# Kernel optimization log

Measured on AMD Instinct MI355X. Metric: run time of the kernel, lower is better.

## Reference

```python
import jax, jax.numpy as jnp
import numpy as np

N_HEAD = 16
D_MODEL = 1024
D_HEAD = 64
B = 2
S = 2048      # query length
M = 512       # memory length
K = S + M     # key length
L = 2 * K - 1 # relative position table length
SCALE = 1.0 / np.sqrt(D_MODEL)  # NOTE: module scales by 1/sqrt(d_model), not d_head
EPS = 1e-5


def layer_norm(x, gamma, beta):
    mu = jnp.mean(x, axis=-1, keepdims=True)
    var = jnp.mean(jnp.square(x - mu), axis=-1, keepdims=True)
    return (x - mu) * jax.lax.rsqrt(var + EPS) * gamma + beta


def skew(qpos, mem_len):
    # qpos: (B, H, S, 2K-1) -> relative-position scores aligned to keys (B, H, S, K)
    b, h, s, l = qpos.shape
    k_len = (l + 1) // 2
    pad = jnp.full((b, h, s, 1), -jnp.inf, dtype=qpos.dtype)
    rel = jnp.concatenate([qpos, pad], axis=-1)          # (B,H,S,2K)
    rel = rel.reshape(b, h, s * (l + 1))[..., : s * l]    # drop tail, shift rows
    rel = rel.reshape(b, h, s, l)
    start = (k_len - 1) - mem_len
    return rel[..., start : start + k_len]


def setup_inputs() -> dict:
    key = jax.random.key(0)
    ks = jax.random.split(key, 8)
    w_scale = 1.0 / np.sqrt(D_MODEL)
    hidden = jax.random.normal(ks[0], (B, S, D_MODEL), jnp.float32)
    memory = jax.random.normal(ks[1], (B, M, D_MODEL), jnp.float32)
    pos_emb = jax.random.normal(ks[2], (B, L, D_HEAD), jnp.float32)
    Wq = jax.random.normal(ks[3], (D_MODEL, N_HEAD * D_HEAD), jnp.float32) * w_scale
    Wk = jax.random.normal(ks[4], (D_MODEL, N_HEAD * D_HEAD), jnp.float32) * w_scale
    Wv = jax.random.normal(ks[5], (D_MODEL, N_HEAD * D_HEAD), jnp.float32) * w_scale
    Wo = jax.random.normal(ks[6], (N_HEAD * D_HEAD, D_MODEL), jnp.float32) * w_scale
    gamma = jnp.ones((D_MODEL,), jnp.float32)
    beta = jnp.zeros((D_MODEL,), jnp.float32)
    # causal mask with memory: query i may attend keys j <= i + M; True = drop
    i = jnp.arange(S)[:, None]
    j = jnp.arange(K)[None, :]
    mask = j > (i + M)  # (S, K) bool
    return {"hidden": hidden, "pos_emb": pos_emb, "memory": memory,
            "Wq": Wq, "Wk": Wk, "Wv": Wv, "Wo": Wo,
            "gamma": gamma, "beta": beta, "mask": mask}


def reference(hidden, pos_emb, memory, Wq, Wk, Wv, Wo, gamma, beta, mask):
    combined = jnp.concatenate([memory, hidden], axis=1)  # (B, K, D)
    hn = layer_norm(hidden, gamma, beta)                  # pre_lnorm
    cn = layer_norm(combined, gamma, beta)
    q = (hn @ Wq).reshape(B, S, N_HEAD, D_HEAD).transpose(0, 2, 1, 3)  # (B,H,S,Dh)
    k = (cn @ Wk).reshape(B, K, N_HEAD, D_HEAD).transpose(0, 2, 1, 3)  # (B,H,K,Dh)
    v = (cn @ Wv).reshape(B, K, N_HEAD, D_HEAD).transpose(0, 2, 1, 3)  # (B,H,K,Dh)
    scores = jnp.einsum("bhsd,bhkd->bhsk", q, k)           # content term
    qpos = jnp.einsum("bhsd,bld->bhsl", q, pos_emb)        # position term (B,H,S,2K-1)
    scores = (scores + skew(qpos, M)) * SCALE
    scores = jnp.where(mask[None, None], -jnp.inf, scores)
    attn = jax.nn.softmax(scores, axis=-1)
    atten_vec = jnp.einsum("bhsk,bhkd->bshd", attn, v).reshape(B, S, N_HEAD * D_HEAD)
    output = atten_vec @ Wo
    # faithful quirk: residual uses the layer-normed hidden when pre_lnorm=True
    return hn + output
```

## Files before the change

### kernel.cpp

```cpp
#include <hip/hip_runtime.h>

typedef unsigned short u16;
typedef float f32x4 __attribute__((ext_vector_type(4)));
typedef short short8 __attribute__((ext_vector_type(8)));

#define MFMA_BF16(a, b, c) __builtin_amdgcn_mfma_f32_16x16x32_bf16((a), (b), (c), 0, 0, 0)

#define NEG_BIG (-30000.0f)

typedef __attribute__((address_space(1))) const void gas_void;
typedef __attribute__((address_space(3))) void las_void;

__device__ __forceinline__ float bf2f(u16 v) {
  union { unsigned int u; float f; } c; c.u = ((unsigned int)v) << 16; return c.f;
}
__device__ __forceinline__ u16 f2bf(float f) {
  union { float f; unsigned int u; } c; c.f = f;
  return (u16)((c.u + 0x7fffu + ((c.u >> 16) & 1u)) >> 16);
}

__global__ __launch_bounds__(256) void cast_pe_k(const float* __restrict__ src, u16* __restrict__ dst,
                                                 int n4, int* __restrict__ ctr) {
  const int idx = blockIdx.x * 256 + threadIdx.x;
  if (idx == 0) *ctr = 0;
  if (idx >= n4) return;
  const float4 d = *(const float4*)&src[idx * 4];
  ushort4 o;
  o.x = f2bf(d.x); o.y = f2bf(d.y); o.z = f2bf(d.z); o.w = f2bf(d.w);
  *(ushort4*)&dst[idx * 4] = o;
}

__global__ __launch_bounds__(256) void transpose_k(const float* __restrict__ W0, const float* __restrict__ W1,
                                                   const float* __restrict__ W2, const float* __restrict__ W3,
                                                   u16* __restrict__ Wt) {
  __shared__ float t[32][33];
  const float* W = (blockIdx.z == 0) ? W0 : (blockIdx.z == 1) ? W1 : (blockIdx.z == 2) ? W2 : W3;
  u16* dst = Wt + (size_t)blockIdx.z * 1024 * 1024;
  const int tx = threadIdx.x, ty = threadIdx.y;
  const int x0 = blockIdx.x * 32, y0 = blockIdx.y * 32;
#pragma unroll
  for (int i = 0; i < 32; i += 8)
    t[ty + i][tx] = W[(size_t)(y0 + ty + i) * 1024 + x0 + tx];
  __syncthreads();
#pragma unroll
  for (int i = 0; i < 32; i += 8)
    dst[(size_t)(x0 + ty + i) * 1024 + y0 + tx] = f2bf(t[tx][ty + i]);
}

__global__ __launch_bounds__(256) void ln_k(const float* __restrict__ hid, const float* __restrict__ mem,
                                            const float* __restrict__ gam, const float* __restrict__ bet,
                                            u16* __restrict__ cn) {
  const int row = blockIdx.x;
  const int b = (row >= 2560) ? 1 : 0;
  const int r = row - b * 2560;
  const float* src = (r < 512) ? (mem + ((size_t)b * 512 + r) * 1024)
                               : (hid + ((size_t)b * 2048 + (r - 512)) * 1024);
  const int tid = threadIdx.x;
  const float4 d = *(const float4*)&src[tid * 4];
  float x[4] = {d.x, d.y, d.z, d.w};
  float s = x[0] + x[1] + x[2] + x[3];
  float q = x[0]*x[0] + x[1]*x[1] + x[2]*x[2] + x[3]*x[3];
#pragma unroll
  for (int o = 1; o < 64; o <<= 1) { s += __shfl_xor(s, o); q += __shfl_xor(q, o); }
  __shared__ float sb[4], qsb[4];
  const int wave = tid >> 6;
  if ((tid & 63) == 0) { sb[wave] = s; qsb[wave] = q; }
  __syncthreads();
  s = sb[0] + sb[1] + sb[2] + sb[3];
  q = qsb[0] + qsb[1] + qsb[2] + qsb[3];
  const float mu = s * (1.0f / 1024.0f);
  const float var = q * (1.0f / 1024.0f) - mu * mu;
  const float rstd = rsqrtf(fmaxf(var, 0.0f) + 1e-5f);
  u16 o4[4];
#pragma unroll
  for (int i = 0; i < 4; ++i) {
    const int c = tid * 4 + i;
    o4[i] = f2bf((x[i] - mu) * rstd * gam[c] + bet[c]);
  }
  uint2 pk;
  pk.x = (unsigned)o4[0] | ((unsigned)o4[1] << 16);
  pk.y = (unsigned)o4[2] | ((unsigned)o4[3] << 16);
  *(uint2*)&cn[((size_t)b * 2560 + r) * 1024 + tid * 4] = pk;
}

__global__ __launch_bounds__(256, 3) void gemm128_k(const u16* __restrict__ A, const u16* __restrict__ Bt,
                                                    u16* __restrict__ qb, u16* __restrict__ kbo,
                                                    u16* __restrict__ vtb) {
  __shared__ u16 smem[16384];
  const int tid = threadIdx.x;
  const int lane = tid & 63, w = tid >> 6;
  const int quad = lane >> 4, l15 = lane & 15, r7 = l15 & 7;
  const int wr = w >> 1, wc = w & 1;
  const int row0 = blockIdx.y * 128, col0 = blockIdx.x * 128;
  const int rloc = w * 8 + (lane >> 3);
  const int cg = ((lane & 7) ^ ((lane >> 3) & 7)) * 8;
  const u16* ga = A + (size_t)(row0 + rloc) * 1024 + cg;
  const u16* gb = Bt + (size_t)(col0 + rloc) * 1024 + cg;
  f32x4 z = {0.f, 0.f, 0.f, 0.f};
  f32x4 acc[4][4];
#pragma unroll
  for (int m = 0; m < 4; ++m)
#pragma unroll
    for (int n = 0; n < 4; ++n) acc[m][n] = z;
  for (int kt = 0; kt < 16; ++kt) {
    const int k0 = kt * 64;
#pragma unroll
    for (int g2 = 0; g2 < 4; ++g2) {
      __builtin_amdgcn_global_load_lds((gas_void*)(ga + (size_t)g2 * 32 * 1024 + k0),
                                       (las_void*)(smem + (g2 * 32 + w * 8) * 64), 16, 0, 0);
      __builtin_amdgcn_global_load_lds((gas_void*)(gb + (size_t)g2 * 32 * 1024 + k0),
                                       (las_void*)(smem + 8192 + (g2 * 32 + w * 8) * 64), 16, 0, 0);
    }
    __syncthreads();
    short8 af0[4], af1[4];
#pragma unroll
    for (int m = 0; m < 4; ++m) {
      const int row = wr * 64 + m * 16 + l15;
      af0[m] = *(const short8*)&smem[row * 64 + (quad ^ r7) * 8];
      af1[m] = *(const short8*)&smem[row * 64 + ((quad + 4) ^ r7) * 8];
    }
#pragma unroll
    for (int n = 0; n < 4; ++n) {
      const int row = wc * 64 + n * 16 + l15;
      const short8 bf0 = *(const short8*)&smem[8192 + row * 64 + (quad ^ r7) * 8];
      const short8 bf1 = *(const short8*)&smem[8192 + row * 64 + ((quad + 4) ^ r7) * 8];
#pragma unroll
      for (int m = 0; m < 4; ++m) {
        acc[m][n] = MFMA_BF16(af0[m], bf0, acc[m][n]);
        acc[m][n] = MFMA_BF16(af1[m], bf1, acc[m][n]);
      }
    }
    __syncthreads();
  }
  const int nc = col0 >> 10;
  if (nc != 2) {
#pragma unroll
    for (int m = 0; m < 4; ++m) {
#pragma unroll
      for (int n = 0; n < 4; ++n) {
#pragma unroll
        for (int r = 0; r < 4; ++r) {
          const int R = row0 + wr * 64 + m * 16 + quad * 4 + r;
          const int C = col0 + wc * 64 + n * 16 + l15;
          const float v = acc[m][n][r];
          const int c = C & 1023, h = c >> 6, dh = c & 63;
          const int b = (R >= 2560) ? 1 : 0, kk = R - b * 2560;
          if (nc == 0) {
            if (kk >= 512)
              qb[(((size_t)(b * 16 + h)) * 2048 + (kk - 512)) * 64 + dh] = f2bf(v * 0.03125f);
          } else {
            kbo[(((size_t)(b * 16 + h)) * 2560 + kk) * 64 + dh] = f2bf(v);
          }
        }
      }
    }
  } else {
#pragma unroll
    for (int m = 0; m < 4; ++m)
#pragma unroll
      for (int n = 0; n < 4; ++n)
#pragma unroll
        for (int r = 0; r < 4; ++r) {
          const int rl = wr * 64 + m * 16 + quad * 4 + r;
          const int cl = wc * 64 + n * 16 + l15;
          smem[cl * 128 + (rl ^ ((cl & 7) << 3))] = f2bf(acc[m][n][r]);
        }
    __syncthreads();
    const int bb = (row0 >= 2560) ? 1 : 0;
    const int kk0 = row0 - bb * 2560;
#pragma unroll
    for (int half = 0; half < 2; ++half) {
      const int cl = (tid >> 2) + half * 64;
      const int c = (col0 - 2048) + cl;
      const int hh = c >> 6, dh = c & 63;
      u16* dst = &vtb[(((size_t)(bb * 16 + hh)) * 64 + dh) * 2560 + kk0];
#pragma unroll
      for (int inner = 0; inner < 4; ++inner) {
        const int rl = inner * 32 + (tid & 3) * 8;
        *(short8*)(dst + rl) = *(const short8*)&smem[cl * 128 + (rl ^ ((cl & 7) << 3))];
      }
    }
  }
}

__global__ __launch_bounds__(256, 3) void gemm_out_k(const u16* __restrict__ A, const u16* __restrict__ Bt,
                                                     float* __restrict__ outf,
                                                     const u16* __restrict__ resid) {
  __shared__ u16 smem[16384];
  const int tid = threadIdx.x;
  const int lane = tid & 63, w = tid >> 6;
  const int quad = lane >> 4, l15 = lane & 15, r7 = l15 & 7;
  const int wr = w >> 1, wc = w & 1;
  const int row0 = blockIdx.y * 128, col0 = blockIdx.x * 128;
  const int rloc = w * 8 + (lane >> 3);
  const int cg = ((lane & 7) ^ ((lane >> 3) & 7)) * 8;
  const u16* ga = A + (size_t)(row0 + rloc) * 1024 + cg;
  const u16* gb = Bt + (size_t)(col0 + rloc) * 1024 + cg;
  f32x4 z = {0.f, 0.f, 0.f, 0.f};
  f32x4 acc[4][4];
#pragma unroll
  for (int m = 0; m < 4; ++m)
#pragma unroll
    for (int n = 0; n < 4; ++n) acc[m][n] = z;
  for (int kt = 0; kt < 16; ++kt) {
    const int k0 = kt * 64;
#pragma unroll
    for (int g2 = 0; g2 < 4; ++g2) {
      __builtin_amdgcn_global_load_lds((gas_void*)(ga + (size_t)g2 * 32 * 1024 + k0),
                                       (las_void*)(smem + (g2 * 32 + w * 8) * 64), 16, 0, 0);
      __builtin_amdgcn_global_load_lds((gas_void*)(gb + (size_t)g2 * 32 * 1024 + k0),
                                       (las_void*)(smem + 8192 + (g2 * 32 + w * 8) * 64), 16, 0, 0);
    }
    __syncthreads();
    short8 af0[4], af1[4];
#pragma unroll
    for (int m = 0; m < 4; ++m) {
      const int row = wr * 64 + m * 16 + l15;
      af0[m] = *(const short8*)&smem[row * 64 + (quad ^ r7) * 8];
      af1[m] = *(const short8*)&smem[row * 64 + ((quad + 4) ^ r7) * 8];
    }
#pragma unroll
    for (int n = 0; n < 4; ++n) {
      const int row = wc * 64 + n * 16 + l15;
      const short8 bf0 = *(const short8*)&smem[8192 + row * 64 + (quad ^ r7) * 8];
      const short8 bf1 = *(const short8*)&smem[8192 + row * 64 + ((quad + 4) ^ r7) * 8];
#pragma unroll
      for (int m = 0; m < 4; ++m) {
        acc[m][n] = MFMA_BF16(af0[m], bf0, acc[m][n]);
        acc[m][n] = MFMA_BF16(af1[m], bf1, acc[m][n]);
      }
    }
    __syncthreads();
  }
#pragma unroll
  for (int m = 0; m < 4; ++m) {
#pragma unroll
    for (int n = 0; n < 4; ++n) {
#pragma unroll
      for (int r = 0; r < 4; ++r) {
        const int R = row0 + wr * 64 + m * 16 + quad * 4 + r;
        const int C = col0 + wc * 64 + n * 16 + l15;
        const size_t rrow = (size_t)(R >> 11) * 2560 + 512 + (R & 2047);
        outf[(size_t)R * 1024 + C] = acc[m][n][r] + bf2f(resid[rrow * 1024 + C]);
      }
    }
  }
}

__global__ __launch_bounds__(512, 4) void attn_k(const u16* __restrict__ q, const u16* __restrict__ kb,
                                                 const u16* __restrict__ vt, const u16* __restrict__ pe,
                                                 u16* __restrict__ p0, u16* __restrict__ p1,
                                                 float* __restrict__ l0, float* __restrict__ l1,
                                                 int* __restrict__ ctr) {
  __shared__ u16 Kt[2][64][64];
  __shared__ u16 Vt[2][64][64];
  __shared__ u16 Pw[8][16][68];
  volatile int* mailbox = (volatile int*)&Pw[0][0][64];
  const int tid = threadIdx.x, lane = tid & 63, wave = tid >> 6;
  const int quad = lane >> 4, l15 = lane & 15, r7 = l15 & 7;
  const int srow = wave * 8 + (lane >> 3);
  const int sch8 = ((lane & 7) ^ ((lane >> 3) & 7)) * 8;
  const f32x4 z = {0.f, 0.f, 0.f, 0.f};
  for (;;) {
    if (tid == 0) *mailbox = atomicAdd(ctr, 1);
    __syncthreads();
    const int item = *mailbox;
    if (item >= 1024) return;
    const int qt = 15 - (item >> 6);
    const int bh = (item & 63) >> 1, half = item & 1;
    const int b = bh >> 4, h = bh & 15;
    const int qi0 = qt * 128 + wave * 16;
    const int nh = qt + 5;
    const int t0 = half * nh, t1 = t0 + nh;
    const u16* qrow = q + ((size_t)bh * 2048 + qi0 + l15) * 64 + quad * 8;
    const short8 aq0 = *(const short8*)qrow;
    const short8 aq1 = *(const short8*)(qrow + 32);
    const u16* kp = kb + ((size_t)bh * 2560 + srow) * 64 + sch8;
    const u16* vp = vt + ((size_t)bh * 64 + srow) * 2560 + sch8;
    const u16* pp = pe + ((long)b * 5119 - qi0 + 2032 + l15) * 64 + quad * 8 + (size_t)t0 * 4096;
    f32x4 acc[4];
#pragma unroll
    for (int i = 0; i < 4; ++i) acc[i] = z;
    float lrow[4] = {0.f, 0.f, 0.f, 0.f};
    const int jlast = qi0 + 527;
    __builtin_amdgcn_global_load_lds((gas_void*)(kp + (size_t)t0 * 4096),
                                     (las_void*)(&Kt[0][wave * 8][0]), 16, 0, 0);
    __builtin_amdgcn_global_load_lds((gas_void*)(vp + t0 * 64),
                                     (las_void*)(&Vt[0][wave * 8][0]), 16, 0, 0);
    __syncthreads();
    for (int jt = t0; jt < t1; ++jt) {
      const int j0 = jt * 64;
      const int cur = (jt - t0) & 1;
      const int jn = (jt + 1 < t1) ? (jt + 1) : jt;
      __builtin_amdgcn_global_load_lds((gas_void*)(kp + (size_t)jn * 4096),
                                       (las_void*)(&Kt[cur ^ 1][wave * 8][0]), 16, 0, 0);
      __builtin_amdgcn_global_load_lds((gas_void*)(vp + jn * 64),
                                       (las_void*)(&Vt[cur ^ 1][wave * 8][0]), 16, 0, 0);
      if (j0 <= jlast) {
        short8 pb[5], pb2[5];
#pragma unroll
        for (int g = 0; g < 5; ++g) {
          pb[g]  = *(const short8*)(pp + 1024 * g);
          pb2[g] = *(const short8*)(pp + 1024 * g + 32);
        }
        f32x4 sc[4];
#pragma unroll
        for (int s = 0; s < 4; ++s) {
          sc[s] = MFMA_BF16(aq0, *(const short8*)&Kt[cur][16 * s + l15][(quad ^ r7) * 8], z);
          sc[s] = MFMA_BF16(aq1, *(const short8*)&Kt[cur][16 * s + l15][((quad + 4) ^ r7) * 8], sc[s]);
        }
        f32x4 qp[5];
#pragma unroll
        for (int g = 0; g < 5; ++g) {
          qp[g] = MFMA_BF16(aq0, pb[g], z);
          qp[g] = MFMA_BF16(aq1, pb2[g], qp[g]);
        }
#pragma unroll
        for (int r = 0; r < 4; ++r) {
          const int di = quad * 4 + r;
          const int o = l15 - di + 15;
          const int src = quad * 16 + (o & 15);
          const float g0 = __shfl(qp[0][r], src);
          const float g1 = __shfl(qp[1][r], src);
          const float g2 = __shfl(qp[2][r], src);
          const float g3 = __shfl(qp[3][r], src);
          const float g4 = __shfl(qp[4][r], src);
          const bool lo = (o < 16);
          float s0 = sc[0][r] + (lo ? g0 : g1);
          float s1 = sc[1][r] + (lo ? g1 : g2);
          float s2 = sc[2][r] + (lo ? g2 : g3);
          float s3 = sc[3][r] + (lo ? g3 : g4);
          const int jlim = qi0 + di + 512 - j0 - l15;
          if (0 > jlim)  s0 = NEG_BIG;
          if (16 > jlim) s1 = NEG_BIG;
          if (32 > jlim) s2 = NEG_BIG;
          if (48 > jlim) s3 = NEG_BIG;
          const float p0v = __expf(s0);
          const float p1v = __expf(s1);
          const float p2v = __expf(s2);
          const float p3v = __expf(s3);
          lrow[r] += (p0v + p1v) + (p2v + p3v);
          Pw[wave][di][l15]      = f2bf(p0v);
          Pw[wave][di][16 + l15] = f2bf(p1v);
          Pw[wave][di][32 + l15] = f2bf(p2v);
          Pw[wave][di][48 + l15] = f2bf(p3v);
        }
        asm volatile("s_waitcnt lgkmcnt(0)" ::: "memory");
        const short8 pf0 = *(const short8*)&Pw[wave][l15][quad * 8];
        const short8 pf1 = *(const short8*)&Pw[wave][l15][32 + quad * 8];
#pragma unroll
        for (int n = 0; n < 4; ++n) {
          acc[n] = MFMA_BF16(pf0, *(const short8*)&Vt[cur][16 * n + l15][(quad ^ r7) * 8], acc[n]);
          acc[n] = MFMA_BF16(pf1, *(const short8*)&Vt[cur][16 * n + l15][((quad + 4) ^ r7) * 8], acc[n]);
        }
      }
      __syncthreads();
      pp += 4096;
    }
    u16* od = half ? p1 : p0;
    float* ol = half ? l1 : l0;
#pragma unroll
    for (int r = 0; r < 4; ++r) {
      float lsum = lrow[r];
#pragma unroll
      for (int o = 1; o < 16; o <<= 1) lsum += __shfl_xor(lsum, o);
      const int s = qi0 + quad * 4 + r;
      if (l15 == 0) ol[(size_t)bh * 2048 + s] = lsum;
#pragma unroll
      for (int n = 0; n < 4; ++n) {
        const int c = h * 64 + n * 16 + l15;
        od[((size_t)b * 2048 + s) * 1024 + c] = f2bf(acc[n][r]);
      }
    }
  }
}

__global__ __launch_bounds__(256) void combine_k(u16* __restrict__ av, const u16* __restrict__ p1,
                                                 const float* __restrict__ l0, const float* __restrict__ l1) {
  const int idx = blockIdx.x * 256 + threadIdx.x;
  const int base = idx * 4;
  const int row = base >> 10;
  const int col = base & 1023;
  const int b = row >> 11, s = row & 2047;
  const int h = col >> 6;
  const size_t li = ((size_t)(b * 16 + h)) * 2048 + s;
  const float inv = 1.0f / (l0[li] + l1[li]);
  const ushort4 a0 = *(const ushort4*)&av[(size_t)base];
  const ushort4 a1 = *(const ushort4*)&p1[(size_t)base];
  ushort4 o;
  o.x = f2bf((bf2f(a0.x) + bf2f(a1.x)) * inv);
  o.y = f2bf((bf2f(a0.y) + bf2f(a1.y)) * inv);
  o.z = f2bf((bf2f(a0.z) + bf2f(a1.z)) * inv);
  o.w = f2bf((bf2f(a0.w) + bf2f(a1.w)) * inv);
  *(ushort4*)&av[(size_t)base] = o;
}

extern "C" void kernel_launch(void* const* d_in, const int* in_sizes, int n_in,
                              void* d_out, int out_size, void* d_ws, size_t ws_size,
                              hipStream_t stream) {
  const float* hidden = (const float*)d_in[0];
  const float* pe     = (const float*)d_in[1];
  const float* memv   = (const float*)d_in[2];
  const float* Wq     = (const float*)d_in[3];
  const float* Wk     = (const float*)d_in[4];
  const float* Wv     = (const float*)d_in[5];
  const float* Wo     = (const float*)d_in[6];
  const float* gam    = (const float*)d_in[7];
  const float* bet    = (const float*)d_in[8];

  u16* ws  = (u16*)d_ws;
  u16* cn  = ws;
  u16* qb  = cn  + (size_t)5120 * 1024;
  u16* kb  = qb  + (size_t)4096 * 1024;
  u16* vt  = kb  + (size_t)5120 * 1024;
  u16* av  = vt  + (size_t)5120 * 1024;
  u16* wt  = av  + (size_t)4096 * 1024;
  u16* peb = wt  + (size_t)4 * 1024 * 1024;
  u16* p1  = peb + (size_t)2 * 5119 * 64;
  float* l0 = (float*)(p1 + (size_t)4096 * 1024);
  float* l1 = l0 + (size_t)32 * 2048;
  int* ctr  = (int*)(l1 + (size_t)32 * 2048);

  const int pe_n4 = (2 * 5119 * 64) / 4;
  cast_pe_k<<<(pe_n4 + 255) / 256, 256, 0, stream>>>(pe, peb, pe_n4, ctr);
  ln_k<<<5120, 256, 0, stream>>>(hidden, memv, gam, bet, cn);
  transpose_k<<<dim3(32, 32, 4), dim3(32, 8), 0, stream>>>(Wq, Wk, Wv, Wo, wt);
  gemm128_k<<<dim3(24, 40), 256, 0, stream>>>(cn, wt, qb, kb, vt);
  attn_k<<<768, 512, 0, stream>>>(qb, kb, vt, peb, av, p1, l0, l1, ctr);
  combine_k<<<4096, 256, 0, stream>>>(av, p1, l0, l1);
  gemm_out_k<<<dim3(8, 32), 256, 0, stream>>>(av, wt + (size_t)3 * 1024 * 1024,
                                              (float*)d_out, cn);
}
```

Before: 313.5 us.

## Merge prep kernels into one launch, fold log2e into Q, pack bf16 conversions

Three prep kernels (positional-embedding cast, layernorm, weight transpose) are combined into one launch that branches on block index, removing two kernel launches and their gaps. The Q scale now also includes log2(e), so the attention softmax can use exp2f in place of __expf. The probability-to-bf16 conversion uses the hardware packed v_cvt_pk_bf16_f32 instruction, which converts two values per instruction instead of the manual rounding. In exchange, the merged kernel has divergent block roles and shared-memory use, and the hardware conversion's rounding may differ slightly from the manual one.

```diff
diff --git a/kernel.cpp b/kernel.cpp
--- a/kernel.cpp
+++ b/kernel.cpp
@@ -7,6 +7,7 @@
 #define MFMA_BF16(a, b, c) __builtin_amdgcn_mfma_f32_16x16x32_bf16((a), (b), (c), 0, 0, 0)
 
 #define NEG_BIG (-30000.0f)
+#define QSCALE (0.03125f * 1.4426950408889634f)
 
 typedef __attribute__((address_space(1))) const void gas_void;
 typedef __attribute__((address_space(3))) void las_void;
@@ -19,68 +20,71 @@
   return (u16)((c.u + 0x7fffu + ((c.u >> 16) & 1u)) >> 16);
 }
 
-__global__ __launch_bounds__(256) void cast_pe_k(const float* __restrict__ src, u16* __restrict__ dst,
-                                                 int n4, int* __restrict__ ctr) {
-  const int idx = blockIdx.x * 256 + threadIdx.x;
-  if (idx == 0) *ctr = 0;
-  if (idx >= n4) return;
-  const float4 d = *(const float4*)&src[idx * 4];
-  ushort4 o;
-  o.x = f2bf(d.x); o.y = f2bf(d.y); o.z = f2bf(d.z); o.w = f2bf(d.w);
-  *(ushort4*)&dst[idx * 4] = o;
-}
-
-__global__ __launch_bounds__(256) void transpose_k(const float* __restrict__ W0, const float* __restrict__ W1,
-                                                   const float* __restrict__ W2, const float* __restrict__ W3,
-                                                   u16* __restrict__ Wt) {
-  __shared__ float t[32][33];
-  const float* W = (blockIdx.z == 0) ? W0 : (blockIdx.z == 1) ? W1 : (blockIdx.z == 2) ? W2 : W3;
-  u16* dst = Wt + (size_t)blockIdx.z * 1024 * 1024;
-  const int tx = threadIdx.x, ty = threadIdx.y;
-  const int x0 = blockIdx.x * 32, y0 = blockIdx.y * 32;
-#pragma unroll
-  for (int i = 0; i < 32; i += 8)
-    t[ty + i][tx] = W[(size_t)(y0 + ty + i) * 1024 + x0 + tx];
-  __syncthreads();
-#pragma unroll
-  for (int i = 0; i < 32; i += 8)
-    dst[(size_t)(x0 + ty + i) * 1024 + y0 + tx] = f2bf(t[tx][ty + i]);
-}
-
-__global__ __launch_bounds__(256) void ln_k(const float* __restrict__ hid, const float* __restrict__ mem,
-                                            const float* __restrict__ gam, const float* __restrict__ bet,
-                                            u16* __restrict__ cn) {
-  const int row = blockIdx.x;
-  const int b = (row >= 2560) ? 1 : 0;
-  const int r = row - b * 2560;
-  const float* src = (r < 512) ? (mem + ((size_t)b * 512 + r) * 1024)
-                               : (hid + ((size_t)b * 2048 + (r - 512)) * 1024);
-  const int tid = threadIdx.x;
-  const float4 d = *(const float4*)&src[tid * 4];
-  float x[4] = {d.x, d.y, d.z, d.w};
-  float s = x[0] + x[1] + x[2] + x[3];
-  float q = x[0]*x[0] + x[1]*x[1] + x[2]*x[2] + x[3]*x[3];
-#pragma unroll
-  for (int o = 1; o < 64; o <<= 1) { s += __shfl_xor(s, o); q += __shfl_xor(q, o); }
-  __shared__ float sb[4], qsb[4];
-  const int wave = tid >> 6;
-  if ((tid & 63) == 0) { sb[wave] = s; qsb[wave] = q; }
-  __syncthreads();
-  s = sb[0] + sb[1] + sb[2] + sb[3];
-  q = qsb[0] + qsb[1] + qsb[2] + qsb[3];
-  const float mu = s * (1.0f / 1024.0f);
-  const float var = q * (1.0f / 1024.0f) - mu * mu;
-  const float rstd = rsqrtf(fmaxf(var, 0.0f) + 1e-5f);
-  u16 o4[4];
-#pragma unroll
-  for (int i = 0; i < 4; ++i) {
-    const int c = tid * 4 + i;
-    o4[i] = f2bf((x[i] - mu) * rstd * gam[c] + bet[c]);
-  }
-  uint2 pk;
-  pk.x = (unsigned)o4[0] | ((unsigned)o4[1] << 16);
-  pk.y = (unsigned)o4[2] | ((unsigned)o4[3] << 16);
-  *(uint2*)&cn[((size_t)b * 2560 + r) * 1024 + tid * 4] = pk;
+__global__ __launch_bounds__(256) void prep_k(const float* __restrict__ pe_src, u16* __restrict__ pe_dst,
+                                              int* __restrict__ ctr,
+                                              const float* __restrict__ hid, const float* __restrict__ mem,
+                                              const float* __restrict__ gam, const float* __restrict__ bet,
+                                              u16* __restrict__ cn,
+                                              const float* __restrict__ W0, const float* __restrict__ W1,
+                                              const float* __restrict__ W2, const float* __restrict__ W3,
+                                              u16* __restrict__ Wt) {
+  __shared__ float shm[32 * 33 + 8];
+  const int bx = blockIdx.x, tid = threadIdx.x;
+  if (bx < 641) {
+    const int idx = bx * 256 + tid;
+    if (idx == 0) *ctr = 0;
+    const int n4 = (2 * 5119 * 64) / 4;
+    if (idx >= n4) return;
+    const float4 d = *(const float4*)&pe_src[idx * 4];
+    ushort4 o;
+    o.x = f2bf(d.x); o.y = f2bf(d.y); o.z = f2bf(d.z); o.w = f2bf(d.w);
+    *(ushort4*)&pe_dst[idx * 4] = o;
+  } else if (bx < 5761) {
+    const int row = bx - 641;
+    const int b = (row >= 2560) ? 1 : 0;
+    const int r = row - b * 2560;
+    const float* src = (r < 512) ? (mem + ((size_t)b * 512 + r) * 1024)
+                                 : (hid + ((size_t)b * 2048 + (r - 512)) * 1024);
+    const float4 d = *(const float4*)&src[tid * 4];
+    float x[4] = {d.x, d.y, d.z, d.w};
+    float s = x[0] + x[1] + x[2] + x[3];
+    float q = x[0]*x[0] + x[1]*x[1] + x[2]*x[2] + x[3]*x[3];
+#pragma unroll
+    for (int o = 1; o < 64; o <<= 1) { s += __shfl_xor(s, o); q += __shfl_xor(q, o); }
+    const int wave = tid >> 6;
+    if ((tid & 63) == 0) { shm[wave] = s; shm[4 + wave] = q; }
+    __syncthreads();
+    s = shm[0] + shm[1] + shm[2] + shm[3];
+    q = shm[4] + shm[5] + shm[6] + shm[7];
+    const float mu = s * (1.0f / 1024.0f);
+    const float var = q * (1.0f / 1024.0f) - mu * mu;
+    const float rstd = rsqrtf(fmaxf(var, 0.0f) + 1e-5f);
+    u16 o4[4];
+#pragma unroll
+    for (int i = 0; i < 4; ++i) {
+      const int c = tid * 4 + i;
+      o4[i] = f2bf((x[i] - mu) * rstd * gam[c] + bet[c]);
+    }
+    uint2 pk;
+    pk.x = (unsigned)o4[0] | ((unsigned)o4[1] << 16);
+    pk.y = (unsigned)o4[2] | ((unsigned)o4[3] << 16);
+    *(uint2*)&cn[((size_t)b * 2560 + r) * 1024 + tid * 4] = pk;
+  } else {
+    const int t = bx - 5761;
+    const int tz = t >> 10, rem = t & 1023;
+    const int by = rem >> 5, bxx = rem & 31;
+    const float* W = (tz == 0) ? W0 : (tz == 1) ? W1 : (tz == 2) ? W2 : W3;
+    u16* dst = Wt + (size_t)tz * 1024 * 1024;
+    const int tx = tid & 31, ty = tid >> 5;
+    const int x0 = bxx * 32, y0 = by * 32;
+#pragma unroll
+    for (int i = 0; i < 32; i += 8)
+      shm[(ty + i) * 33 + tx] = W[(size_t)(y0 + ty + i) * 1024 + x0 + tx];
+    __syncthreads();
+#pragma unroll
+    for (int i = 0; i < 32; i += 8)
+      dst[(size_t)(x0 + ty + i) * 1024 + y0 + tx] = f2bf(shm[tx * 33 + ty + i]);
+  }
 }
 
 __global__ __launch_bounds__(256, 3) void gemm128_k(const u16* __restrict__ A, const u16* __restrict__ Bt,
@@ -147,7 +151,7 @@
           const int b = (R >= 2560) ? 1 : 0, kk = R - b * 2560;
           if (nc == 0) {
             if (kk >= 512)
-              qb[(((size_t)(b * 16 + h)) * 2048 + (kk - 512)) * 64 + dh] = f2bf(v * 0.03125f);
+              qb[(((size_t)(b * 16 + h)) * 2048 + (kk - 512)) * 64 + dh] = f2bf(v * QSCALE);
           } else {
             kbo[(((size_t)(b * 16 + h)) * 2560 + kk) * 64 + dh] = f2bf(v);
           }
@@ -335,15 +339,18 @@
           if (16 > jlim) s1 = NEG_BIG;
           if (32 > jlim) s2 = NEG_BIG;
           if (48 > jlim) s3 = NEG_BIG;
-          const float p0v = __expf(s0);
-          const float p1v = __expf(s1);
-          const float p2v = __expf(s2);
-          const float p3v = __expf(s3);
+          const float p0v = exp2f(s0);
+          const float p1v = exp2f(s1);
+          const float p2v = exp2f(s2);
+          const float p3v = exp2f(s3);
           lrow[r] += (p0v + p1v) + (p2v + p3v);
-          Pw[wave][di][l15]      = f2bf(p0v);
-          Pw[wave][di][16 + l15] = f2bf(p1v);
-          Pw[wave][di][32 + l15] = f2bf(p2v);
-          Pw[wave][di][48 + l15] = f2bf(p3v);
+          unsigned pk01, pk23;
+          asm("v_cvt_pk_bf16_f32 %0, %1, %2" : "=v"(pk01) : "v"(p0v), "v"(p1v));
+          asm("v_cvt_pk_bf16_f32 %0, %1, %2" : "=v"(pk23) : "v"(p2v), "v"(p3v));
+          Pw[wave][di][l15]      = (u16)pk01;
+          Pw[wave][di][16 + l15] = (u16)(pk01 >> 16);
+          Pw[wave][di][32 + l15] = (u16)pk23;
+          Pw[wave][di][48 + l15] = (u16)(pk23 >> 16);
         }
         asm volatile("s_waitcnt lgkmcnt(0)" ::: "memory");
         const short8 pf0 = *(const short8*)&Pw[wave][l15][quad * 8];
@@ -421,10 +428,8 @@
   float* l1 = l0 + (size_t)32 * 2048;
   int* ctr  = (int*)(l1 + (size_t)32 * 2048);
 
-  const int pe_n4 = (2 * 5119 * 64) / 4;
-  cast_pe_k<<<(pe_n4 + 255) / 256, 256, 0, stream>>>(pe, peb, pe_n4, ctr);
-  ln_k<<<5120, 256, 0, stream>>>(hidden, memv, gam, bet, cn);
-  transpose_k<<<dim3(32, 32, 4), dim3(32, 8), 0, stream>>>(Wq, Wk, Wv, Wo, wt);
+  prep_k<<<9857, 256, 0, stream>>>(pe, peb, ctr, hidden, memv, gam, bet, cn,
+                                   Wq, Wk, Wv, Wo, wt);
   gemm128_k<<<dim3(24, 40), 256, 0, stream>>>(cn, wt, qb, kb, vt);
   attn_k<<<768, 512, 0, stream>>>(qb, kb, vt, peb, av, p1, l0, l1, ctr);
   combine_k<<<4096, 256, 0, stream>>>(av, p1, l0, l1);
```

After: 343.6 us. +9.6%, slower.
